# Performance work log

Hardware: AMD Instinct MI355X
Metric: run time of the kernel (lower is better)

## Reference

```python
import jax, jax.numpy as jnp
import numpy as np

MS = 64  # matrixSize
POOL_W = 256  # AdaptiveMaxPool2d target width


def _conv(x, w, b, stride):
    y = jax.lax.conv_general_dilated(x, w, (stride, stride), ((1, 1), (1, 1)),
                                     dimension_numbers=('NCHW', 'OIHW', 'NCHW'))
    return y + b[None, :, None, None]


def _image_cnn(x, c1w, c1b, c2w, c2b, c3w, c3b, fcw, fcb, fg):
    f = jax.nn.relu(_conv(x, c1w, c1b, 2))
    f = jax.nn.relu(_conv(f, c2w, c2b, 2))
    f = _conv(f, c3w, c3b, 2)                 # [1,16,h,w]
    c = f.shape[1]
    feat = f.reshape(c, -1)                    # [16, h*w]
    sel = feat[:, fg]                          # masked gather -> [16, K]
    K = sel.shape[1]
    # AdaptiveMaxPool2d((16,256)) on [1,16,K]: H 16->16 identity, W K->256 with K%256==0
    pooled = sel.reshape(c, POOL_W, K // POOL_W).max(axis=2)
    return pooled.reshape(1, -1) @ fcw.T + fcb  # [1, MS*MS]


def _forward(cF, sF, content, style,
             snet_c1_w, snet_c1_b, snet_c2_w, snet_c2_b, snet_c3_w, snet_c3_b, snet_fc_w, snet_fc_b,
             cnet_c1_w, cnet_c1_b, cnet_c2_w, cnet_c2_b, cnet_c3_w, cnet_c3_b, cnet_fc_w, cnet_fc_b,
             compress_w, compress_b, unzip_w, unzip_b, fgcmask, fgsmask):
    # per-sample style/content transform matrices
    sMat = _image_cnn(style, snet_c1_w, snet_c1_b, snet_c2_w, snet_c2_b,
                      snet_c3_w, snet_c3_b, snet_fc_w, snet_fc_b, fgsmask).reshape(MS, MS)
    cMat = _image_cnn(content, cnet_c1_w, cnet_c1_b, cnet_c2_w, cnet_c2_b,
                      cnet_c3_w, cnet_c3_b, cnet_fc_w, cnet_fc_b, fgcmask).reshape(MS, MS)
    T = sMat @ cMat                            # [MS, MS]

    b, _, h, w = cF.shape
    # 1x1 conv compress: 512 -> MS
    cc = jnp.einsum('oc,bchw->bohw', compress_w.reshape(MS, -1), cF) + compress_b[None, :, None, None]
    ccf = cc.reshape(MS, h * w)
    ccf = ccf - ccf.mean(axis=1, keepdims=True)   # subtract mean over ALL pixels
    transFG = T @ ccf[:, fgcmask]                 # transform foreground columns [MS, K]
    tf = ccf.at[:, fgcmask].set(transFG)          # scatter back (index_copy_)
    # 1x1 conv unzip: MS -> 512
    out = jnp.einsum('oc,bchw->bohw', unzip_w.reshape(-1, MS), tf.reshape(b, MS, h, w)) + unzip_b[None, :, None, None]
    return out


def setup_inputs() -> dict:
    key = jax.random.key(0)
    ks = jax.random.split(key, 32)
    rn = lambda k, shape, s: jax.random.normal(k, shape, jnp.float32) * s
    H, h, K = 1024, 128, 8192
    inp = {
        'cF': rn(ks[0], (1, 512, h, h), 1.0),
        'sF': rn(ks[1], (1, 512, h, h), 1.0),
        'content': rn(ks[2], (1, 3, H, H), 1.0),
        'style': rn(ks[3], (1, 3, H, H), 1.0),
    }
    i = 4
    for net in ('snet', 'cnet'):
        specs = [('c1_w', (64, 3, 3, 3), 0.1), ('c1_b', (64,), 0.01),
                 ('c2_w', (32, 64, 3, 3), 0.05), ('c2_b', (32,), 0.01),
                 ('c3_w', (16, 32, 3, 3), 0.05), ('c3_b', (16,), 0.01),
                 ('fc_w', (MS * MS, 16 * POOL_W), 0.02), ('fc_b', (MS * MS,), 0.01)]
        for name, shape, s in specs:
            inp[f'{net}_{name}'] = rn(ks[i], shape, s); i += 1
    inp['compress_w'] = rn(ks[i], (MS, 512, 1, 1), 0.05); i += 1
    inp['compress_b'] = rn(ks[i], (MS,), 0.01); i += 1
    inp['unzip_w'] = rn(ks[i], (512, MS, 1, 1), 0.05); i += 1
    inp['unzip_b'] = rn(ks[i], (512,), 0.01); i += 1
    inp['fgcmask'] = jnp.sort(jax.random.randint(ks[i], (K,), 0, h * h, dtype=jnp.int32)); i += 1
    inp['fgsmask'] = jnp.sort(jax.random.randint(ks[i], (K,), 0, h * h, dtype=jnp.int32))
    return inp


def reference(cF, sF, content, style,
              snet_c1_w, snet_c1_b, snet_c2_w, snet_c2_b, snet_c3_w, snet_c3_b, snet_fc_w, snet_fc_b,
              cnet_c1_w, cnet_c1_b, cnet_c2_w, cnet_c2_b, cnet_c3_w, cnet_c3_b, cnet_fc_w, cnet_fc_b,
              compress_w, compress_b, unzip_w, unzip_b, fgcmask, fgsmask):
    return _forward(cF, sF, content, style,
                    snet_c1_w, snet_c1_b, snet_c2_w, snet_c2_b, snet_c3_w, snet_c3_b, snet_fc_w, snet_fc_b,
                    cnet_c1_w, cnet_c1_b, cnet_c2_w, cnet_c2_b, cnet_c3_w, cnet_c3_b, cnet_fc_w, cnet_fc_b,
                    compress_w, compress_b, unzip_w, unzip_b, fgcmask, fgsmask)
```

## Files before the change

### kernel.cpp

```cpp
#include <hip/hip_runtime.h>
#include <hip/hip_bf16.h>

typedef __hip_bfloat16 bf16;

__device__ __forceinline__ float b2f(bf16 v) { return __bfloat162float(v); }
__device__ __forceinline__ bf16  f2b(float v) { return __float2bfloat16(v); }
__device__ __forceinline__ float blo(unsigned u) { return __uint_as_float(u << 16); }
__device__ __forceinline__ float bhi(unsigned u) { return __uint_as_float(u & 0xffff0000u); }

template<int F32>
__device__ __forceinline__ float ldin(const void* p, size_t i) {
  if (F32) return ((const float*)p)[i];
  return b2f(((const bf16*)p)[i]);
}
__device__ __forceinline__ float ldrt(const void* p, size_t i, int f) {
  return f ? ((const float*)p)[i] : b2f(((const bf16*)p)[i]);
}

__global__ void k_detect(const unsigned short* __restrict__ u, int* __restrict__ flag)
{
  const int lane = threadIdx.x;
  int nb = 0;
  #pragma unroll
  for (int t = 0; t < 4; t++) {
    unsigned e = (u[lane * 4 + t] >> 7) & 0xFFu;
    nb += (e >= 0x90u) ? 1 : 0;
  }
  #pragma unroll
  for (int off = 32; off > 0; off >>= 1) nb += __shfl_down(nb, off);
  if (lane == 0) flag[0] = (nb > 8) ? 1 : 0;
}

__global__ __launch_bounds__(256) void k_prep(
    const void* __restrict__ s_w1, const void* __restrict__ s_b1,
    const void* __restrict__ s_w2, const void* __restrict__ s_b2,
    const void* __restrict__ s_w3, const void* __restrict__ s_b3,
    const void* __restrict__ c_w1, const void* __restrict__ c_b1,
    const void* __restrict__ c_w2, const void* __restrict__ c_b2,
    const void* __restrict__ c_w3, const void* __restrict__ c_b3,
    float* __restrict__ w1f, float* __restrict__ b1f,
    float* __restrict__ w2f, float* __restrict__ b2f,
    float* __restrict__ w3f, float* __restrict__ b3f,
    const int* __restrict__ flag)
{
  const int f = flag[0];
  int t = blockIdx.x * 256 + threadIdx.x;
  if (t >= 49760) return;
  const int net = (t >= 24880) ? 1 : 0;
  int r = t - net * 24880;
  const void* W1 = net ? c_w1 : s_w1;  const void* B1 = net ? c_b1 : s_b1;
  const void* W2 = net ? c_w2 : s_w2;  const void* B2 = net ? c_b2 : s_b2;
  const void* W3 = net ? c_w3 : s_w3;  const void* B3 = net ? c_b3 : s_b3;
  if (r < 1728) {
    int k = r >> 6, ch = r & 63;
    w1f[net * 1728 + r] = ldrt(W1, (size_t)ch * 27 + k, f);
    return;
  }
  r -= 1728;
  if (r < 64) { b1f[net * 64 + r] = ldrt(B1, r, f); return; }
  r -= 64;
  if (r < 18432) {
    int oc = r & 31, kk = r >> 5;
    w2f[net * 18432 + r] = ldrt(W2, (size_t)oc * 576 + kk, f);
    return;
  }
  r -= 18432;
  if (r < 32) { b2f[net * 32 + r] = ldrt(B2, r, f); return; }
  r -= 32;
  if (r < 4608) {
    int oc = r & 15, kk = r >> 4;
    w3f[net * 4608 + r] = ldrt(W3, (size_t)oc * 288 + kk, f);
    return;
  }
  r -= 4608;
  b3f[net * 16 + r] = ldrt(B3, r, f);
}

struct SmConv12 {
  bf16  ins[3][35][68];
  bf16  c1s[8][17][40];
  alignas(16) float w1a[27][64];
};

template<int F32>
__device__ __forceinline__ void conv12_body(
    const void* __restrict__ IN, const float* __restrict__ w1f_net,
    const float* __restrict__ b1f_net, const float* __restrict__ w2f_net,
    const float* __restrict__ b2f_net, bf16* __restrict__ OUT, SmConv12& sm)
{
  const int tid = threadIdx.x;
  const int R0 = blockIdx.y << 3;
  const int C0 = blockIdx.x << 4;

  const int ibr = 4 * R0 - 3, ibc = 4 * C0 - 3;
  for (int i = tid; i < 7140; i += 256) {
    int ch  = i / 2380;
    int rem = i - ch * 2380;
    int li = rem / 68, lc = rem - li * 68;
    int iy = ibr + li, ix = ibc + lc;
    float v = 0.f;
    if ((unsigned)iy < 1024u && (unsigned)ix < 1024u)
      v = ldin<F32>(IN, (size_t)ch * 1048576 + (size_t)iy * 1024 + ix);
    sm.ins[ch][li][lc] = f2b(v);
  }
  for (int i = tid; i < 1728; i += 256)
    (&sm.w1a[0][0])[i] = w1f_net[i];
  __syncthreads();

  const int og  = tid >> 7;
  const int ogu = __builtin_amdgcn_readfirstlane(og);
  const int p  = tid & 127;
  const int r  = p >> 4;
  const int c  = p & 15;

  float acc[16];
  #pragma unroll
  for (int j = 0; j < 16; j++) acc[j] = b2f_net[ogu * 16 + j];

  #pragma unroll 1
  for (int ss = 0; ss < 8; ss++) {
    if (ss) __syncthreads();
    const int ss8 = ss * 8;

    float bb[8];
    #pragma unroll
    for (int ch = 0; ch < 8; ch++) bb[ch] = b1f_net[ss8 + ch];

    for (int i = tid; i < 561; i += 256) {
      const int lr = i / 33, lc = i - lr * 33;
      const int g1r = 2 * R0 - 1 + lr, g1c = 2 * C0 - 1 + lc;
      if (((unsigned)g1r < 512u) && ((unsigned)g1c < 512u)) {
        float a1[8];
        #pragma unroll
        for (int ch = 0; ch < 8; ch++) a1[ch] = bb[ch];
        #pragma unroll
        for (int ic = 0; ic < 3; ic++) {
          #pragma unroll
          for (int ky = 0; ky < 3; ky++) {
            const int* rp = (const int*)&sm.ins[ic][2 * lr + ky][0];
            const unsigned u0 = (unsigned)rp[lc];
            const unsigned u1 = (unsigned)rp[lc + 1];
            const float v3[3] = { blo(u0), bhi(u0), blo(u1) };
            #pragma unroll
            for (int kx = 0; kx < 3; kx++) {
              const int k = ic * 9 + ky * 3 + kx;
              const float4 wA = *(const float4*)&sm.w1a[k][ss8];
              const float4 wB = *(const float4*)&sm.w1a[k][ss8 + 4];
              const float v = v3[kx];
              a1[0] += wA.x * v; a1[1] += wA.y * v;
              a1[2] += wA.z * v; a1[3] += wA.w * v;
              a1[4] += wB.x * v; a1[5] += wB.y * v;
              a1[6] += wB.z * v; a1[7] += wB.w * v;
            }
          }
        }
        #pragma unroll
        for (int ch = 0; ch < 8; ch++)
          sm.c1s[ch][lr][lc] = f2b(fmaxf(a1[ch], 0.f));
      } else {
        #pragma unroll
        for (int ch = 0; ch < 8; ch++) sm.c1s[ch][lr][lc] = f2b(0.f);
      }
    }
    __syncthreads();

    const float* __restrict__ W2F = w2f_net + (size_t)ss * 72 * 32 + ogu * 16;
    #pragma unroll
    for (int icl = 0; icl < 8; icl++) {
      float cv[3][3];
      #pragma unroll
      for (int ky = 0; ky < 3; ky++) {
        const int* cp = (const int*)&sm.c1s[icl][2 * r + ky][0];
        const unsigned u0 = (unsigned)cp[c];
        const unsigned u1 = (unsigned)cp[c + 1];
        cv[ky][0] = blo(u0); cv[ky][1] = bhi(u0); cv[ky][2] = blo(u1);
      }
      #pragma unroll
      for (int ky = 0; ky < 3; ky++) {
        #pragma unroll
        for (int kx = 0; kx < 3; kx++) {
          const int kk = icl * 9 + ky * 3 + kx;
          const float v = cv[ky][kx];
          const float* wr = W2F + kk * 32;
          #pragma unroll
          for (int j4 = 0; j4 < 4; j4++) {
            const float4 w4 = *(const float4*)&wr[j4 * 4];
            acc[j4 * 4 + 0] += w4.x * v; acc[j4 * 4 + 1] += w4.y * v;
            acc[j4 * 4 + 2] += w4.z * v; acc[j4 * 4 + 3] += w4.w * v;
          }
        }
      }
    }
  }

  const size_t sp = (size_t)(R0 + r) * 256 + (C0 + c);
  #pragma unroll
  for (int j = 0; j < 16; j++)
    OUT[(size_t)(og * 16 + j) * 65536 + sp] = f2b(fmaxf(acc[j], 0.f));
}

__global__ __launch_bounds__(256) void k_conv12(
    const void* __restrict__ in0, const void* __restrict__ in1,
    const float* __restrict__ w1f, const float* __restrict__ b1f,
    const float* __restrict__ w2f, const float* __restrict__ b2f,
    bf16* __restrict__ c2o, const int* __restrict__ flag)
{
  __shared__ SmConv12 sm;
  const int n = blockIdx.z;
  const void* IN = n ? in1 : in0;
  const float* W1 = w1f + n * 1728;
  const float* B1 = b1f + n * 64;
  const float* W2 = w2f + n * 18432;
  const float* B2 = b2f + n * 32;
  bf16* OUT = c2o + (size_t)n * 2097152;
  if (flag[0]) conv12_body<1>(IN, W1, B1, W2, B2, OUT, sm);
  else         conv12_body<0>(IN, W1, B1, W2, B2, OUT, sm);
}

__global__ __launch_bounds__(256) void k_conv3(
    const bf16* __restrict__ in,
    const float* __restrict__ w3f, const float* __restrict__ b3f,
    float* __restrict__ out)
{
  const int n = blockIdx.z;
  const bf16* __restrict__ IN = in + (size_t)n * 32 * 65536;
  const int ocg = __builtin_amdgcn_readfirstlane(blockIdx.y);
  const float* __restrict__ WF = w3f + (size_t)n * 4608 + ocg * 4;
  const int tid = threadIdx.x;
  const int s = blockIdx.x * 256 + tid;
  const int oy = s >> 7, ox = s & 127;
  float acc[4];
  #pragma unroll
  for (int j = 0; j < 4; j++) acc[j] = b3f[n * 16 + ocg * 4 + j];
  #pragma unroll 2
  for (int ic = 0; ic < 32; ic++) {
    const int* __restrict__ I32 = (const int*)(IN + (size_t)ic * 65536);
    #pragma unroll
    for (int ky = 0; ky < 3; ky++) {
      const int iy = 2 * oy + ky - 1;
      const bool oky = (unsigned)iy < 256u;
      const int rb = iy * 128;
      const unsigned um = (oky && ox > 0) ? (unsigned)I32[rb + ox - 1] : 0u;
      const unsigned u0 = oky ? (unsigned)I32[rb + ox] : 0u;
      const float v3[3] = { bhi(um), blo(u0), bhi(u0) };
      #pragma unroll
      for (int kx = 0; kx < 3; kx++) {
        const int kk = ic * 9 + ky * 3 + kx;
        const float4 w4 = *(const float4*)&WF[kk * 16];
        const float v = v3[kx];
        acc[0] += w4.x * v; acc[1] += w4.y * v;
        acc[2] += w4.z * v; acc[3] += w4.w * v;
      }
    }
  }
  float* O = out + (size_t)n * 16 * 16384;
  #pragma unroll
  for (int j = 0; j < 4; j++) O[(size_t)(ocg * 4 + j) * 16384 + s] = acc[j];
}

__global__ __launch_bounds__(256) void k_pool(
    const float* __restrict__ feat,
    const int* __restrict__ fgs, const int* __restrict__ fgc,
    float* __restrict__ pooled)
{
  int t = blockIdx.x * 256 + threadIdx.x;
  int n = t >> 12, rem = t & 4095;
  int c = rem >> 8, p = rem & 255;
  const int* __restrict__ m = n ? fgc : fgs;
  const float* __restrict__ F = feat + (size_t)n * 16 * 16384 + (size_t)c * 16384;
  float mx = -3.4e38f;
  #pragma unroll 4
  for (int j = 0; j < 32; j++) mx = fmaxf(mx, F[m[p * 32 + j]]);
  pooled[(size_t)n * 4096 + rem] = mx;
}

__global__ __launch_bounds__(256) void k_fc(
    const float* __restrict__ pooled,
    const void* __restrict__ w0, const void* __restrict__ bb0,
    const void* __restrict__ w1, const void* __restrict__ bb1,
    float* __restrict__ mats, const int* __restrict__ flag)
{
  __shared__ float red[4];
  const int n = blockIdx.z;
  const int i = blockIdx.x;
  const void* W = n ? w1  : w0;
  const void* B = n ? bb1 : bb0;
  const float* __restrict__ P = pooled + (size_t)n * 4096;
  const int tid = threadIdx.x;
  const int f = flag[0];

  const float4* P4 = (const float4*)(P + (size_t)tid * 16);
  const float4 p0 = P4[0], p1 = P4[1], p2 = P4[2], p3 = P4[3];
  float p;
  if (f) {
    const float4* W4 = (const float4*)((const float*)W + (size_t)i * 4096 + tid * 16);
    const float4 w0v = W4[0], w1v = W4[1], w2v = W4[2], w3v = W4[3];
    p = w0v.x*p0.x + w0v.y*p0.y + w0v.z*p0.z + w0v.w*p0.w
      + w1v.x*p1.x + w1v.y*p1.y + w1v.z*p1.z + w1v.w*p1.w
      + w2v.x*p2.x + w2v.y*p2.y + w2v.z*p2.z + w2v.w*p2.w
      + w3v.x*p3.x + w3v.y*p3.y + w3v.z*p3.z + w3v.w*p3.w;
  } else {
    const int4* Wb = (const int4*)((const bf16*)W + (size_t)i * 4096 + tid * 16);
    const int4 a = Wb[0], b = Wb[1];
    p = blo((unsigned)a.x)*p0.x + bhi((unsigned)a.x)*p0.y
      + blo((unsigned)a.y)*p0.z + bhi((unsigned)a.y)*p0.w
      + blo((unsigned)a.z)*p1.x + bhi((unsigned)a.z)*p1.y
      + blo((unsigned)a.w)*p1.z + bhi((unsigned)a.w)*p1.w
      + blo((unsigned)b.x)*p2.x + bhi((unsigned)b.x)*p2.y
      + blo((unsigned)b.y)*p2.z + bhi((unsigned)b.y)*p2.w
      + blo((unsigned)b.z)*p3.x + bhi((unsigned)b.z)*p3.y
      + blo((unsigned)b.w)*p3.z + bhi((unsigned)b.w)*p3.w;
  }
  #pragma unroll
  for (int off = 32; off > 0; off >>= 1) p += __shfl_down(p, off);
  if ((tid & 63) == 0) red[tid >> 6] = p;
  __syncthreads();
  if (tid == 0) {
    float b = f ? ((const float*)B)[i] : b2f(((const bf16*)B)[i]);
    mats[(size_t)n * 4096 + i] = red[0] + red[1] + red[2] + red[3] + b;
  }
}

__global__ __launch_bounds__(256) void k_tmat(
    const float* __restrict__ mats, float* __restrict__ T)
{
  int t = blockIdx.x * 256 + threadIdx.x;
  int i = t >> 6, j = t & 63;
  const float* __restrict__ S = mats;
  const float* __restrict__ C = mats + 4096;
  float a = 0.f;
  #pragma unroll 8
  for (int k = 0; k < 64; k++) a += S[i * 64 + k] * C[k * 64 + j];
  T[t] = a;
}

struct SmComp {
  alignas(16) float wl[512][20];
  alignas(16) float red[128][17];
  float bl[16];
};

template<int F32>
__device__ __forceinline__ void compress_body(
    const void* __restrict__ cF, const void* __restrict__ cw,
    const void* __restrict__ cb, float* __restrict__ ccf, SmComp& sm)
{
  const int og = blockIdx.y;
  const int tid = threadIdx.x;
  for (int i = tid; i < 8192; i += 256) {
    int ol = i >> 9, ch = i & 511;
    sm.wl[ch][ol] = ldin<F32>(cw, (size_t)(og * 16 + ol) * 512 + ch);
  }
  if (tid < 16) sm.bl[tid] = ldin<F32>(cb, og * 16 + tid);
  __syncthreads();

  const int sl   = tid & 127;
  const int half = tid >> 7;
  const int s = blockIdx.x * 128 + sl;
  float acc[16];
  #pragma unroll
  for (int j = 0; j < 16; j++) acc[j] = half ? 0.f : sm.bl[j];
  const int c0 = half * 256;
  #pragma unroll 4
  for (int ci = 0; ci < 256; ci++) {
    const int ch = c0 + ci;
    float v = ldin<F32>(cF, (size_t)ch * 16384 + s);
    #pragma unroll
    for (int j4 = 0; j4 < 4; j4++) {
      const float4 w4 = *(const float4*)&sm.wl[ch][j4 * 4];
      acc[j4 * 4 + 0] += w4.x * v; acc[j4 * 4 + 1] += w4.y * v;
      acc[j4 * 4 + 2] += w4.z * v; acc[j4 * 4 + 3] += w4.w * v;
    }
  }
  if (half) {
    #pragma unroll
    for (int j = 0; j < 16; j++) sm.red[sl][j] = acc[j];
  }
  __syncthreads();
  if (!half) {
    #pragma unroll
    for (int j = 0; j < 16; j++)
      ccf[(size_t)(og * 16 + j) * 16384 + s] = acc[j] + sm.red[sl][j];
  }
}

__global__ __launch_bounds__(256) void k_compress(
    const void* __restrict__ cF, const void* __restrict__ cw,
    const void* __restrict__ cb, float* __restrict__ ccf,
    const int* __restrict__ flag)
{
  __shared__ SmComp sm;
  if (flag[0]) compress_body<1>(cF, cw, cb, ccf, sm);
  else         compress_body<0>(cF, cw, cb, ccf, sm);
}

__global__ __launch_bounds__(256) void k_mean(
    const float* __restrict__ ccf, float* __restrict__ mean)
{
  const int o = blockIdx.x;
  const int tid = threadIdx.x;
  __shared__ float red[256];
  const float* __restrict__ R = ccf + (size_t)o * 16384;
  float p = 0.f;
  for (int s = tid; s < 16384; s += 256) p += R[s];
  red[tid] = p;
  __syncthreads();
  for (int off = 128; off > 0; off >>= 1) {
    if (tid < off) red[tid] += red[tid + off];
    __syncthreads();
  }
  if (tid == 0) mean[o] = red[0] * (1.f / 16384.f);
}

__global__ __launch_bounds__(256) void k_scatter(
    const int* __restrict__ fgc, int* __restrict__ maskf)
{
  int t = blockIdx.x * 256 + threadIdx.x;
  maskf[fgc[t]] = 1;
}

__global__ __launch_bounds__(256) void k_transform(
    const float* __restrict__ ccf, const float* __restrict__ Tm,
    const float* __restrict__ mean, const int* __restrict__ maskf,
    bf16* __restrict__ tf)
{
  const int og = blockIdx.y;
  __shared__ __align__(16) float Tl[8][64];
  __shared__ float ml[64];
  const int tid = threadIdx.x;
  for (int i = tid; i < 512; i += 256) {
    int ol = i >> 6, op = i & 63;
    Tl[ol][op] = Tm[(size_t)(og * 8 + ol) * 64 + op];
  }
  if (tid < 64) ml[tid] = mean[tid];
  __syncthreads();
  const int s = blockIdx.x * 256 + tid;
  const bool msk = maskf[s] != 0;
  float col[64];
  #pragma unroll
  for (int op = 0; op < 64; op++) col[op] = ccf[(size_t)op * 16384 + s] - ml[op];
  #pragma unroll
  for (int ol = 0; ol < 8; ol++) {
    float a = 0.f;
    #pragma unroll
    for (int op4 = 0; op4 < 16; op4++) {
      float4 t4 = *(const float4*)&Tl[ol][op4 * 4];
      a += t4.x * col[op4 * 4 + 0] + t4.y * col[op4 * 4 + 1]
         + t4.z * col[op4 * 4 + 2] + t4.w * col[op4 * 4 + 3];
    }
    const int row = og * 8 + ol;
    tf[(size_t)row * 16384 + s] = f2b(msk ? a : col[row]);
  }
}

struct SmUnzip { alignas(16) float wl[64][32]; float bl[32]; };

template<int F32>
__device__ __forceinline__ void unzip_body(
    const bf16* __restrict__ tf, const void* __restrict__ uw,
    const void* __restrict__ ub, void* __restrict__ outp, SmUnzip& sm)
{
  const int ug = blockIdx.y;
  const int tid = threadIdx.x;
  for (int i = tid; i < 2048; i += 256) {
    int ul = i & 31, o = i >> 5;
    sm.wl[o][ul] = ldin<F32>(uw, (size_t)(ug * 32 + ul) * 64 + o);
  }
  if (tid < 32) sm.bl[tid] = ldin<F32>(ub, ug * 32 + tid);
  __syncthreads();
  const int s = blockIdx.x * 256 + tid;
  float acc[32];
  #pragma unroll
  for (int j = 0; j < 32; j++) acc[j] = sm.bl[j];
  #pragma unroll 4
  for (int o = 0; o < 64; o++) {
    float v = b2f(tf[(size_t)o * 16384 + s]);
    #pragma unroll
    for (int j4 = 0; j4 < 8; j4++) {
      const float4 w4 = *(const float4*)&sm.wl[o][j4 * 4];
      acc[j4 * 4 + 0] += w4.x * v; acc[j4 * 4 + 1] += w4.y * v;
      acc[j4 * 4 + 2] += w4.z * v; acc[j4 * 4 + 3] += w4.w * v;
    }
  }
  #pragma unroll
  for (int j = 0; j < 32; j++) {
    size_t idx = (size_t)(ug * 32 + j) * 16384 + s;
    if (F32) ((float*)outp)[idx] = acc[j];
    else     ((bf16*)outp)[idx]  = f2b(acc[j]);
  }
}

__global__ __launch_bounds__(256) void k_unzip(
    const bf16* __restrict__ tf,
    const void* __restrict__ uw, const void* __restrict__ ub,
    void* __restrict__ outp, const int* __restrict__ flag)
{
  __shared__ SmUnzip sm;
  if (flag[0]) unzip_body<1>(tf, uw, ub, outp, sm);
  else         unzip_body<0>(tf, uw, ub, outp, sm);
}

extern "C" void kernel_launch(void* const* d_in, const int* in_sizes, int n_in,
                              void* d_out, int out_size, void* d_ws, size_t ws_size,
                              hipStream_t stream)
{
  const void* cF      = d_in[0];
  const void* content = d_in[2];
  const void* style   = d_in[3];
  const void* s_c1w = d_in[4];  const void* s_c1b = d_in[5];
  const void* s_c2w = d_in[6];  const void* s_c2b = d_in[7];
  const void* s_c3w = d_in[8];  const void* s_c3b = d_in[9];
  const void* s_fcw = d_in[10]; const void* s_fcb = d_in[11];
  const void* c_c1w = d_in[12]; const void* c_c1b = d_in[13];
  const void* c_c2w = d_in[14]; const void* c_c2b = d_in[15];
  const void* c_c3w = d_in[16]; const void* c_c3b = d_in[17];
  const void* c_fcw = d_in[18]; const void* c_fcb = d_in[19];
  const void* cw = d_in[20];    const void* cb = d_in[21];
  const void* uw = d_in[22];    const void* ub = d_in[23];
  const int* fgc = (const int*)d_in[24];
  const int* fgs = (const int*)d_in[25];
  (void)in_sizes; (void)n_in; (void)out_size; (void)ws_size;

  char* ob = (char*)d_out;
  bf16*  c2o    = (bf16*)(ob + 0);
  float* c3o    = (float*)(ob + 8388608);
  float* ccf    = (float*)(ob + 10485760);
  float* pooled = (float*)(ob + 14680064);
  float* mats   = (float*)(ob + 14712832);
  float* T      = (float*)(ob + 14745600);
  float* mean   = (float*)(ob + 14761984);
  int*   maskf  = (int*)(ob + 14763008);
  int*   flag   = (int*)(ob + 14828544);
  float* w2f    = (float*)(ob + 14829568);
  float* w1f    = (float*)(ob + 14977024);
  float* w3f    = (float*)(ob + 14990848);
  float* b1f    = (float*)(ob + 15027712);
  float* b2f    = (float*)(ob + 15028224);
  float* b3f    = (float*)(ob + 15028480);

  bf16* tf = (bf16*)d_ws;

  k_detect<<<1, 64, 0, stream>>>((const unsigned short*)cF, flag);
  k_prep<<<195, 256, 0, stream>>>(
      s_c1w, s_c1b, s_c2w, s_c2b, s_c3w, s_c3b,
      c_c1w, c_c1b, c_c2w, c_c2b, c_c3w, c_c3b,
      w1f, b1f, w2f, b2f, w3f, b3f, flag);
  (void)hipMemsetAsync(maskf, 0, 16384 * sizeof(int), stream);
  k_scatter<<<32, 256, 0, stream>>>(fgc, maskf);

  k_conv12<<<dim3(16, 32, 2), 256, 0, stream>>>(
      style, content, w1f, b1f, w2f, b2f, c2o, flag);

  k_conv3<<<dim3(64, 4, 2), 256, 0, stream>>>(c2o, w3f, b3f, c3o);
  k_pool<<<32, 256, 0, stream>>>(c3o, fgs, fgc, pooled);
  k_fc<<<dim3(4096, 1, 2), 256, 0, stream>>>(pooled, s_fcw, s_fcb, c_fcw, c_fcb, mats, flag);
  k_tmat<<<16, 256, 0, stream>>>(mats, T);

  k_compress<<<dim3(128, 4), 256, 0, stream>>>(cF, cw, cb, ccf, flag);
  k_mean<<<64, 256, 0, stream>>>(ccf, mean);
  k_transform<<<dim3(64, 8), 256, 0, stream>>>(ccf, T, mean, maskf, tf);
  k_unzip<<<dim3(64, 16), 256, 0, stream>>>(tf, uw, ub, d_out, flag);
}
```

Measured before the change: 512.5 us.

## Fuse small launches: merge detect/scatter into prep, conv3 with compress, tmat into transform

```diff
diff --git a/kernel.cpp b/kernel.cpp
--- a/kernel.cpp
+++ b/kernel.cpp
@@ -17,63 +17,82 @@
   return f ? ((const float*)p)[i] : b2f(((const bf16*)p)[i]);
 }
 
-__global__ void k_detect(const unsigned short* __restrict__ u, int* __restrict__ flag)
-{
-  const int lane = threadIdx.x;
-  int nb = 0;
-  #pragma unroll
-  for (int t = 0; t < 4; t++) {
-    unsigned e = (u[lane * 4 + t] >> 7) & 0xFFu;
-    nb += (e >= 0x90u) ? 1 : 0;
-  }
-  #pragma unroll
-  for (int off = 32; off > 0; off >>= 1) nb += __shfl_down(nb, off);
-  if (lane == 0) flag[0] = (nb > 8) ? 1 : 0;
-}
-
 __global__ __launch_bounds__(256) void k_prep(
+    const unsigned short* __restrict__ cFu,
     const void* __restrict__ s_w1, const void* __restrict__ s_b1,
     const void* __restrict__ s_w2, const void* __restrict__ s_b2,
     const void* __restrict__ s_w3, const void* __restrict__ s_b3,
     const void* __restrict__ c_w1, const void* __restrict__ c_b1,
     const void* __restrict__ c_w2, const void* __restrict__ c_b2,
     const void* __restrict__ c_w3, const void* __restrict__ c_b3,
+    const void* __restrict__ cw,  const void* __restrict__ cb,
+    const int* __restrict__ fgc,
     float* __restrict__ w1f, float* __restrict__ b1f,
     float* __restrict__ w2f, float* __restrict__ b2f,
     float* __restrict__ w3f, float* __restrict__ b3f,
-    const int* __restrict__ flag)
-{
-  const int f = flag[0];
-  int t = blockIdx.x * 256 + threadIdx.x;
-  if (t >= 49760) return;
-  const int net = (t >= 24880) ? 1 : 0;
-  int r = t - net * 24880;
-  const void* W1 = net ? c_w1 : s_w1;  const void* B1 = net ? c_b1 : s_b1;
-  const void* W2 = net ? c_w2 : s_w2;  const void* B2 = net ? c_b2 : s_b2;
-  const void* W3 = net ? c_w3 : s_w3;  const void* B3 = net ? c_b3 : s_b3;
-  if (r < 1728) {
-    int k = r >> 6, ch = r & 63;
-    w1f[net * 1728 + r] = ldrt(W1, (size_t)ch * 27 + k, f);
+    float* __restrict__ cwf, float* __restrict__ cbf,
+    int* __restrict__ maskf, int* __restrict__ flag)
+{
+  __shared__ int sflag;
+  const int tid = threadIdx.x;
+  if (tid < 64) {
+    int nb = 0;
+    #pragma unroll
+    for (int t = 0; t < 4; t++) {
+      unsigned e = (cFu[tid * 4 + t] >> 7) & 0xFFu;
+      nb += (e >= 0x90u) ? 1 : 0;
+    }
+    #pragma unroll
+    for (int off = 32; off > 0; off >>= 1) nb += __shfl_down(nb, off);
+    if (tid == 0) sflag = (nb > 8) ? 1 : 0;
+  }
+  __syncthreads();
+  const int f = sflag;
+  const int t = blockIdx.x * 256 + tid;
+  if (blockIdx.x == 0 && tid == 0) flag[0] = f;
+  if (t >= 90784) return;
+
+  if (t < 49760) {
+    const int net = (t >= 24880) ? 1 : 0;
+    int r = t - net * 24880;
+    const void* W1 = net ? c_w1 : s_w1;  const void* B1 = net ? c_b1 : s_b1;
+    const void* W2 = net ? c_w2 : s_w2;  const void* B2 = net ? c_b2 : s_b2;
+    const void* W3 = net ? c_w3 : s_w3;  const void* B3 = net ? c_b3 : s_b3;
+    if (r < 1728) {
+      int k = r >> 6, ch = r & 63;
+      w1f[net * 1728 + r] = ldrt(W1, (size_t)ch * 27 + k, f);
+      return;
+    }
+    r -= 1728;
+    if (r < 64) { b1f[net * 64 + r] = ldrt(B1, r, f); return; }
+    r -= 64;
+    if (r < 18432) {
+      int oc = r & 31, kk = r >> 5;
+      w2f[net * 18432 + r] = ldrt(W2, (size_t)oc * 576 + kk, f);
+      return;
+    }
+    r -= 18432;
+    if (r < 32) { b2f[net * 32 + r] = ldrt(B2, r, f); return; }
+    r -= 32;
+    if (r < 4608) {
+      int oc = r & 15, kk = r >> 4;
+      w3f[net * 4608 + r] = ldrt(W3, (size_t)oc * 288 + kk, f);
+      return;
+    }
+    r -= 4608;
+    b3f[net * 16 + r] = ldrt(B3, r, f);
     return;
   }
-  r -= 1728;
-  if (r < 64) { b1f[net * 64 + r] = ldrt(B1, r, f); return; }
+  int r = t - 49760;
+  if (r < 32768) {
+    int ch = r >> 6, oc = r & 63;
+    cwf[r] = ldrt(cw, (size_t)oc * 512 + ch, f);
+    return;
+  }
+  r -= 32768;
+  if (r < 64) { cbf[r] = ldrt(cb, r, f); return; }
   r -= 64;
-  if (r < 18432) {
-    int oc = r & 31, kk = r >> 5;
-    w2f[net * 18432 + r] = ldrt(W2, (size_t)oc * 576 + kk, f);
-    return;
-  }
-  r -= 18432;
-  if (r < 32) { b2f[net * 32 + r] = ldrt(B2, r, f); return; }
-  r -= 32;
-  if (r < 4608) {
-    int oc = r & 15, kk = r >> 4;
-    w3f[net * 4608 + r] = ldrt(W3, (size_t)oc * 288 + kk, f);
-    return;
-  }
-  r -= 4608;
-  b3f[net * 16 + r] = ldrt(B3, r, f);
+  maskf[fgc[r]] = 1;
 }
 
 struct SmConv12 {
@@ -217,45 +236,107 @@
   else         conv12_body<0>(IN, W1, B1, W2, B2, OUT, sm);
 }
 
-__global__ __launch_bounds__(256) void k_conv3(
-    const bf16* __restrict__ in,
+template<int F32>
+__device__ __forceinline__ void compress_part(
+    const void* __restrict__ cF, const float* __restrict__ cwf,
+    const float* __restrict__ cbf, float* __restrict__ ccf,
+    float* __restrict__ meanRaw, int b, int tid, float (*red)[17])
+{
+  const int og = __builtin_amdgcn_readfirstlane(b >> 7);
+  const int sx = b & 127;
+  const int sl = tid & 127, half = tid >> 7;
+  const int halfu = __builtin_amdgcn_readfirstlane(half);
+  const int s = sx * 128 + sl;
+  float acc[16];
+  #pragma unroll
+  for (int j = 0; j < 16; j++) acc[j] = half ? 0.f : cbf[og * 16 + j];
+  const float* __restrict__ WB = cwf + (size_t)halfu * 256 * 64 + og * 16;
+  #pragma unroll 4
+  for (int ci = 0; ci < 256; ci++) {
+    const int ch = halfu * 256 + ci;
+    const float v = ldin<F32>(cF, (size_t)ch * 16384 + s);
+    const float* wr = WB + ci * 64;
+    #pragma unroll
+    for (int j4 = 0; j4 < 4; j4++) {
+      const float4 w4 = *(const float4*)&wr[j4 * 4];
+      acc[j4 * 4 + 0] += w4.x * v; acc[j4 * 4 + 1] += w4.y * v;
+      acc[j4 * 4 + 2] += w4.z * v; acc[j4 * 4 + 3] += w4.w * v;
+    }
+  }
+  if (half) {
+    #pragma unroll
+    for (int j = 0; j < 16; j++) red[sl][j] = acc[j];
+  }
+  __syncthreads();
+  if (!half) {
+    float fin[16];
+    #pragma unroll
+    for (int j = 0; j < 16; j++) fin[j] = acc[j] + red[sl][j];
+    #pragma unroll
+    for (int j = 0; j < 16; j++)
+      ccf[(size_t)(og * 16 + j) * 16384 + s] = fin[j];
+    const int lane = tid & 63;
+    #pragma unroll
+    for (int j = 0; j < 16; j++) {
+      float rr = fin[j];
+      #pragma unroll
+      for (int off = 32; off > 0; off >>= 1) rr += __shfl_down(rr, off);
+      if (lane == 0) atomicAdd(&meanRaw[og * 16 + j], rr);
+    }
+  }
+}
+
+__global__ __launch_bounds__(256) void k_c3cmp(
+    const bf16* __restrict__ c2o,
     const float* __restrict__ w3f, const float* __restrict__ b3f,
-    float* __restrict__ out)
-{
-  const int n = blockIdx.z;
-  const bf16* __restrict__ IN = in + (size_t)n * 32 * 65536;
-  const int ocg = __builtin_amdgcn_readfirstlane(blockIdx.y);
-  const float* __restrict__ WF = w3f + (size_t)n * 4608 + ocg * 4;
+    float* __restrict__ c3o,
+    const void* __restrict__ cF, const float* __restrict__ cwf,
+    const float* __restrict__ cbf, float* __restrict__ ccf,
+    float* __restrict__ meanRaw, const int* __restrict__ flag)
+{
+  __shared__ float red[128][17];
+  const int bx = blockIdx.x;
   const int tid = threadIdx.x;
-  const int s = blockIdx.x * 256 + tid;
-  const int oy = s >> 7, ox = s & 127;
-  float acc[4];
-  #pragma unroll
-  for (int j = 0; j < 4; j++) acc[j] = b3f[n * 16 + ocg * 4 + j];
-  #pragma unroll 2
-  for (int ic = 0; ic < 32; ic++) {
-    const int* __restrict__ I32 = (const int*)(IN + (size_t)ic * 65536);
-    #pragma unroll
-    for (int ky = 0; ky < 3; ky++) {
-      const int iy = 2 * oy + ky - 1;
-      const bool oky = (unsigned)iy < 256u;
-      const int rb = iy * 128;
-      const unsigned um = (oky && ox > 0) ? (unsigned)I32[rb + ox - 1] : 0u;
-      const unsigned u0 = oky ? (unsigned)I32[rb + ox] : 0u;
-      const float v3[3] = { bhi(um), blo(u0), bhi(u0) };
+  if (bx < 512) {
+    const int n = bx >> 8;
+    const int ocg = __builtin_amdgcn_readfirstlane((bx >> 6) & 3);
+    const int sx = bx & 63;
+    const bf16* __restrict__ IN = c2o + (size_t)n * 32 * 65536;
+    const float* __restrict__ WF = w3f + (size_t)n * 4608 + ocg * 4;
+    const int s = sx * 256 + tid;
+    const int oy = s >> 7, ox = s & 127;
+    float acc[4];
+    #pragma unroll
+    for (int j = 0; j < 4; j++) acc[j] = b3f[n * 16 + ocg * 4 + j];
+    #pragma unroll 2
+    for (int ic = 0; ic < 32; ic++) {
+      const int* __restrict__ I32 = (const int*)(IN + (size_t)ic * 65536);
       #pragma unroll
-      for (int kx = 0; kx < 3; kx++) {
-        const int kk = ic * 9 + ky * 3 + kx;
-        const float4 w4 = *(const float4*)&WF[kk * 16];
-        const float v = v3[kx];
-        acc[0] += w4.x * v; acc[1] += w4.y * v;
-        acc[2] += w4.z * v; acc[3] += w4.w * v;
+      for (int ky = 0; ky < 3; ky++) {
+        const int iy = 2 * oy + ky - 1;
+        const bool oky = (unsigned)iy < 256u;
+        const int rb = iy * 128;
+        const unsigned um = (oky && ox > 0) ? (unsigned)I32[rb + ox - 1] : 0u;
+        const unsigned u0 = oky ? (unsigned)I32[rb + ox] : 0u;
+        const float v3[3] = { bhi(um), blo(u0), bhi(u0) };
+        #pragma unroll
+        for (int kx = 0; kx < 3; kx++) {
+          const int kk = ic * 9 + ky * 3 + kx;
+          const float4 w4 = *(const float4*)&WF[kk * 16];
+          const float v = v3[kx];
+          acc[0] += w4.x * v; acc[1] += w4.y * v;
+          acc[2] += w4.z * v; acc[3] += w4.w * v;
+        }
       }
     }
-  }
-  float* O = out + (size_t)n * 16 * 16384;
-  #pragma unroll
-  for (int j = 0; j < 4; j++) O[(size_t)(ocg * 4 + j) * 16384 + s] = acc[j];
+    float* O = c3o + (size_t)n * 16 * 16384;
+    #pragma unroll
+    for (int j = 0; j < 4; j++) O[(size_t)(ocg * 4 + j) * 16384 + s] = acc[j];
+    return;
+  }
+  const int b = bx - 512;
+  if (flag[0]) compress_part<1>(cF, cwf, cbf, ccf, meanRaw, b, tid, red);
+  else         compress_part<0>(cF, cwf, cbf, ccf, meanRaw, b, tid, red);
 }
 
 __global__ __launch_bounds__(256) void k_pool(
@@ -321,118 +402,28 @@
   }
 }
 
-__global__ __launch_bounds__(256) void k_tmat(
-    const float* __restrict__ mats, float* __restrict__ T)
-{
-  int t = blockIdx.x * 256 + threadIdx.x;
-  int i = t >> 6, j = t & 63;
-  const float* __restrict__ S = mats;
-  const float* __restrict__ C = mats + 4096;
-  float a = 0.f;
-  #pragma unroll 8
-  for (int k = 0; k < 64; k++) a += S[i * 64 + k] * C[k * 64 + j];
-  T[t] = a;
-}
-
-struct SmComp {
-  alignas(16) float wl[512][20];
-  alignas(16) float red[128][17];
-  float bl[16];
-};
-
-template<int F32>
-__device__ __forceinline__ void compress_body(
-    const void* __restrict__ cF, const void* __restrict__ cw,
-    const void* __restrict__ cb, float* __restrict__ ccf, SmComp& sm)
-{
-  const int og = blockIdx.y;
-  const int tid = threadIdx.x;
-  for (int i = tid; i < 8192; i += 256) {
-    int ol = i >> 9, ch = i & 511;
-    sm.wl[ch][ol] = ldin<F32>(cw, (size_t)(og * 16 + ol) * 512 + ch);
-  }
-  if (tid < 16) sm.bl[tid] = ldin<F32>(cb, og * 16 + tid);
-  __syncthreads();
-
-  const int sl   = tid & 127;
-  const int half = tid >> 7;
-  const int s = blockIdx.x * 128 + sl;
-  float acc[16];
-  #pragma unroll
-  for (int j = 0; j < 16; j++) acc[j] = half ? 0.f : sm.bl[j];
-  const int c0 = half * 256;
-  #pragma unroll 4
-  for (int ci = 0; ci < 256; ci++) {
-    const int ch = c0 + ci;
-    float v = ldin<F32>(cF, (size_t)ch * 16384 + s);
-    #pragma unroll
-    for (int j4 = 0; j4 < 4; j4++) {
-      const float4 w4 = *(const float4*)&sm.wl[ch][j4 * 4];
-      acc[j4 * 4 + 0] += w4.x * v; acc[j4 * 4 + 1] += w4.y * v;
-      acc[j4 * 4 + 2] += w4.z * v; acc[j4 * 4 + 3] += w4.w * v;
-    }
-  }
-  if (half) {
-    #pragma unroll
-    for (int j = 0; j < 16; j++) sm.red[sl][j] = acc[j];
-  }
-  __syncthreads();
-  if (!half) {
-    #pragma unroll
-    for (int j = 0; j < 16; j++)
-      ccf[(size_t)(og * 16 + j) * 16384 + s] = acc[j] + sm.red[sl][j];
-  }
-}
-
-__global__ __launch_bounds__(256) void k_compress(
-    const void* __restrict__ cF, const void* __restrict__ cw,
-    const void* __restrict__ cb, float* __restrict__ ccf,
-    const int* __restrict__ flag)
-{
-  __shared__ SmComp sm;
-  if (flag[0]) compress_body<1>(cF, cw, cb, ccf, sm);
-  else         compress_body<0>(cF, cw, cb, ccf, sm);
-}
-
-__global__ __launch_bounds__(256) void k_mean(
-    const float* __restrict__ ccf, float* __restrict__ mean)
-{
-  const int o = blockIdx.x;
-  const int tid = threadIdx.x;
-  __shared__ float red[256];
-  const float* __restrict__ R = ccf + (size_t)o * 16384;
-  float p = 0.f;
-  for (int s = tid; s < 16384; s += 256) p += R[s];
-  red[tid] = p;
-  __syncthreads();
-  for (int off = 128; off > 0; off >>= 1) {
-    if (tid < off) red[tid] += red[tid + off];
-    __syncthreads();
-  }
-  if (tid == 0) mean[o] = red[0] * (1.f / 16384.f);
-}
-
-__global__ __launch_bounds__(256) void k_scatter(
-    const int* __restrict__ fgc, int* __restrict__ maskf)
-{
-  int t = blockIdx.x * 256 + threadIdx.x;
-  maskf[fgc[t]] = 1;
-}
-
 __global__ __launch_bounds__(256) void k_transform(
-    const float* __restrict__ ccf, const float* __restrict__ Tm,
-    const float* __restrict__ mean, const int* __restrict__ maskf,
+    const float* __restrict__ ccf, const float* __restrict__ mats,
+    const float* __restrict__ meanRaw, const int* __restrict__ maskf,
     bf16* __restrict__ tf)
 {
   const int og = blockIdx.y;
   __shared__ __align__(16) float Tl[8][64];
   __shared__ float ml[64];
   const int tid = threadIdx.x;
-  for (int i = tid; i < 512; i += 256) {
-    int ol = i >> 6, op = i & 63;
-    Tl[ol][op] = Tm[(size_t)(og * 8 + ol) * 64 + op];
-  }
-  if (tid < 64) ml[tid] = mean[tid];
+  const float* __restrict__ S = mats;
+  const float* __restrict__ C = mats + 4096;
+  #pragma unroll
+  for (int u = 0; u < 2; u++) {
+    const int idx = tid + u * 256;
+    const int row = idx >> 6, col = idx & 63;
+    const float* Sr = S + (size_t)(og * 8 + row) * 64;
+    float a = 0.f;
+    #pragma unroll 8
+    for (int k = 0; k < 64; k++) a += Sr[k] * C[k * 64 + col];
+    Tl[row][col] = a;
+  }
+  if (tid < 64) ml[tid] = meanRaw[tid] * (1.f / 16384.f);
   __syncthreads();
   const int s = blockIdx.x * 256 + tid;
   const bool msk = maskf[s] != 0;
@@ -453,20 +444,34 @@
   }
 }
 
-struct SmUnzip { alignas(16) float wl[64][32]; float bl[32]; };
-
-template<int F32>
-__device__ __forceinline__ void unzip_body(
+struct SmUnzip { alignas(16) float wl[64][32]; float bl[32]; int f; };
+
+__global__ __launch_bounds__(256) void k_unzip(
     const bf16* __restrict__ tf, const void* __restrict__ uw,
-    const void* __restrict__ ub, void* __restrict__ outp, SmUnzip& sm)
-{
+    const void* __restrict__ ub, void* __restrict__ outp,
+    const unsigned short* __restrict__ cFu)
+{
+  __shared__ SmUnzip sm;
+  const int tid = threadIdx.x;
+  if (tid < 64) {
+    int nb = 0;
+    #pragma unroll
+    for (int t = 0; t < 4; t++) {
+      unsigned e = (cFu[tid * 4 + t] >> 7) & 0xFFu;
+      nb += (e >= 0x90u) ? 1 : 0;
+    }
+    #pragma unroll
+    for (int off = 32; off > 0; off >>= 1) nb += __shfl_down(nb, off);
+    if (tid == 0) sm.f = (nb > 8) ? 1 : 0;
+  }
+  __syncthreads();
+  const int f = sm.f;
   const int ug = blockIdx.y;
-  const int tid = threadIdx.x;
   for (int i = tid; i < 2048; i += 256) {
     int ul = i & 31, o = i >> 5;
-    sm.wl[o][ul] = ldin<F32>(uw, (size_t)(ug * 32 + ul) * 64 + o);
-  }
-  if (tid < 32) sm.bl[tid] = ldin<F32>(ub, ug * 32 + tid);
+    sm.wl[o][ul] = ldrt(uw, (size_t)(ug * 32 + ul) * 64 + o, f);
+  }
+  if (tid < 32) sm.bl[tid] = ldrt(ub, ug * 32 + tid, f);
   __syncthreads();
   const int s = blockIdx.x * 256 + tid;
   float acc[32];
@@ -474,7 +479,7 @@
   for (int j = 0; j < 32; j++) acc[j] = sm.bl[j];
   #pragma unroll 4
   for (int o = 0; o < 64; o++) {
-    float v = b2f(tf[(size_t)o * 16384 + s]);
+    const float v = b2f(tf[(size_t)o * 16384 + s]);
     #pragma unroll
     for (int j4 = 0; j4 < 8; j4++) {
       const float4 w4 = *(const float4*)&sm.wl[o][j4 * 4];
@@ -482,22 +487,17 @@
       acc[j4 * 4 + 2] += w4.z * v; acc[j4 * 4 + 3] += w4.w * v;
     }
   }
-  #pragma unroll
-  for (int j = 0; j < 32; j++) {
-    size_t idx = (size_t)(ug * 32 + j) * 16384 + s;
-    if (F32) ((float*)outp)[idx] = acc[j];
-    else     ((bf16*)outp)[idx]  = f2b(acc[j]);
-  }
-}
-
-__global__ __launch_bounds__(256) void k_unzip(
-    const bf16* __restrict__ tf,
-    const void* __restrict__ uw, const void* __restrict__ ub,
-    void* __restrict__ outp, const int* __restrict__ flag)
-{
-  __shared__ SmUnzip sm;
-  if (flag[0]) unzip_body<1>(tf, uw, ub, outp, sm);
-  else         unzip_body<0>(tf, uw, ub, outp, sm);
+  if (f) {
+    float* O = (float*)outp;
+    #pragma unroll
+    for (int j = 0; j < 32; j++)
+      O[(size_t)(ug * 32 + j) * 16384 + s] = acc[j];
+  } else {
+    bf16* O = (bf16*)outp;
+    #pragma unroll
+    for (int j = 0; j < 32; j++)
+      O[(size_t)(ug * 32 + j) * 16384 + s] = f2b(acc[j]);
+  }
 }
 
 extern "C" void kernel_launch(void* const* d_in, const int* in_sizes, int n_in,
@@ -522,42 +522,38 @@
   (void)in_sizes; (void)n_in; (void)out_size; (void)ws_size;
 
   char* ob = (char*)d_out;
-  bf16*  c2o    = (bf16*)(ob + 0);
-  float* c3o    = (float*)(ob + 8388608);
-  float* ccf    = (float*)(ob + 10485760);
-  float* pooled = (float*)(ob + 14680064);
-  float* mats   = (float*)(ob + 14712832);
-  float* T      = (float*)(ob + 14745600);
-  float* mean   = (float*)(ob + 14761984);
-  int*   maskf  = (int*)(ob + 14763008);
-  int*   flag   = (int*)(ob + 14828544);
-  float* w2f    = (float*)(ob + 14829568);
-  float* w1f    = (float*)(ob + 14977024);
-  float* w3f    = (float*)(ob + 14990848);
-  float* b1f    = (float*)(ob + 15027712);
-  float* b2f    = (float*)(ob + 15028224);
-  float* b3f    = (float*)(ob + 15028480);
+  bf16*  c2o     = (bf16*)(ob + 0);
+  float* c3o     = (float*)(ob + 8388608);
+  float* ccf     = (float*)(ob + 10485760);
+  float* pooled  = (float*)(ob + 14680064);
+  float* mats    = (float*)(ob + 14712832);
+  int*   maskf   = (int*)(ob + 14745600);
+  float* meanRaw = (float*)(ob + 14811136);
+  int*   flag    = (int*)(ob + 14812160);
+  float* w1f     = (float*)(ob + 14812416);
+  float* b1f     = (float*)(ob + 14826240);
+  float* w2f     = (float*)(ob + 14826752);
+  float* b2f     = (float*)(ob + 14974208);
+  float* w3f     = (float*)(ob + 14974464);
+  float* b3f     = (float*)(ob + 15011328);
+  float* cwf     = (float*)(ob + 15011456);
+  float* cbf     = (float*)(ob + 15142528);
 
   bf16* tf = (bf16*)d_ws;
 
-  k_detect<<<1, 64, 0, stream>>>((const unsigned short*)cF, flag);
-  k_prep<<<195, 256, 0, stream>>>(
+  (void)hipMemsetAsync(maskf, 0, 65792, stream);
+  k_prep<<<355, 256, 0, stream>>>(
+      (const unsigned short*)cF,
       s_c1w, s_c1b, s_c2w, s_c2b, s_c3w, s_c3b,
       c_c1w, c_c1b, c_c2w, c_c2b, c_c3w, c_c3b,
-      w1f, b1f, w2f, b2f, w3f, b3f, flag);
-  (void)hipMemsetAsync(maskf, 0, 16384 * sizeof(int), stream);
-  k_scatter<<<32, 256, 0, stream>>>(fgc, maskf);
-
+      cw, cb, fgc,
+      w1f, b1f, w2f, b2f, w3f, b3f, cwf, cbf, maskf, flag);
   k_conv12<<<dim3(16, 32, 2), 256, 0, stream>>>(
       style, content, w1f, b1f, w2f, b2f, c2o, flag);
-
-  k_conv3<<<dim3(64, 4, 2), 256, 0, stream>>>(c2o, w3f, b3f, c3o);
+  k_c3cmp<<<1024, 256, 0, stream>>>(c2o, w3f, b3f, c3o,
+                                    cF, cwf, cbf, ccf, meanRaw, flag);
   k_pool<<<32, 256, 0, stream>>>(c3o, fgs, fgc, pooled);
   k_fc<<<dim3(4096, 1, 2), 256, 0, stream>>>(pooled, s_fcw, s_fcb, c_fcw, c_fcb, mats, flag);
-  k_tmat<<<16, 256, 0, stream>>>(mats, T);
-
-  k_compress<<<dim3(128, 4), 256, 0, stream>>>(cF, cw, cb, ccf, flag);
-  k_mean<<<64, 256, 0, stream>>>(ccf, mean);
-  k_transform<<<dim3(64, 8), 256, 0, stream>>>(ccf, T, mean, maskf, tf);
-  k_unzip<<<dim3(64, 16), 256, 0, stream>>>(tf, uw, ub, d_out, flag);
-}
+  k_transform<<<dim3(64, 8), 256, 0, stream>>>(ccf, mats, meanRaw, maskf, tf);
+  k_unzip<<<dim3(64, 16), 256, 0, stream>>>(tf, uw, ub, d_out, (const unsigned short*)cF);
+}
```

Result: slower. 554.2 us (+8.1%).
